# Kernel tuning notes

Hardware: AMD Instinct MI355X
Metric: run time of the kernel (lower is better)

The kernel has to match this reference:

```python
import jax, jax.numpy as jnp
import numpy as np

LOG_2PI = float(np.log(2.0 * np.pi))


def setup_inputs() -> dict:
    key = jax.random.key(0)
    k1, k2, k3 = jax.random.split(key, 3)
    B, C, D = 256, 1000, 256
    return {
        "x": jax.random.normal(k1, (B, D), dtype=jnp.float32),
        "metric_tensor": jax.random.normal(k2, (B, D, D), dtype=jnp.float32),
        "log_priors": jnp.zeros((C,), dtype=jnp.float32),
        "class_means": jax.random.normal(k3, (C, D), dtype=jnp.float32),
        "class_log_vars": jnp.zeros((C, D), dtype=jnp.float32),
    }


def reference(x, metric_tensor, log_priors, class_means, class_log_vars):
    D = x.shape[-1]
    # diff: [B, C, D]
    diff = x[:, None, :] - class_means[None, :, :]
    # Mahalanobis quadratic form per (batch, class): diff^T G diff
    maha = jnp.einsum("bcd,bde,bce->bc", diff, metric_tensor, diff)
    log_likelihood = -0.5 * (maha + jnp.sum(class_log_vars, axis=-1)[None, :] + D * LOG_2PI)
    log_posteriors = log_likelihood + log_priors[None, :]
    return jax.nn.log_softmax(log_posteriors, axis=-1)
```

## Files before the change

kernel.cpp:

```cpp
#include <hip/hip_runtime.h>

#define LOG2PI 1.83787706640934548356f

typedef __attribute__((ext_vector_type(4))) float f32x4;
typedef __attribute__((ext_vector_type(2))) float f32x2;
typedef __attribute__((ext_vector_type(8))) short bf16x8;

__device__ __forceinline__ unsigned short f2bf(float f) {
    union { float f; unsigned u; } v; v.f = f;
    unsigned r = v.u + 0x7fffu + ((v.u >> 16) & 1u);
    return (unsigned short)(r >> 16);
}
__device__ __forceinline__ float bf2f(unsigned short h) {
    union { unsigned u; float f; } v; v.u = ((unsigned)h) << 16; return v.f;
}
__device__ __forceinline__ bf16x8 pack8(f32x4 a, f32x4 b) {
    bf16x8 h;
    h[0]=(short)f2bf(a[0]); h[1]=(short)f2bf(a[1]); h[2]=(short)f2bf(a[2]); h[3]=(short)f2bf(a[3]);
    h[4]=(short)f2bf(b[0]); h[5]=(short)f2bf(b[1]); h[6]=(short)f2bf(b[2]); h[7]=(short)f2bf(b[3]);
    return h;
}
__device__ __forceinline__ float rowsum16(float v) {
    v += __int_as_float(__builtin_amdgcn_update_dpp(0, __float_as_int(v), 0x111, 0xf, 0xf, true));
    v += __int_as_float(__builtin_amdgcn_update_dpp(0, __float_as_int(v), 0x112, 0xf, 0xf, true));
    v += __int_as_float(__builtin_amdgcn_update_dpp(0, __float_as_int(v), 0x114, 0xf, 0xf, true));
    v += __int_as_float(__builtin_amdgcn_update_dpp(0, __float_as_int(v), 0x118, 0xf, 0xf, true));
    return v;
}

__global__ __launch_bounds__(256)
void k_prep(const float* __restrict__ clv, const float* __restrict__ lp,
            float* __restrict__ bias)
{
    const int w = threadIdx.x >> 6, lane = threadIdx.x & 63;
    const int c = blockIdx.x * 4 + w;
    if (c >= 1000) return;
    f32x4 v = *reinterpret_cast<const f32x4*>(clv + c * 256 + lane * 4);
    float s = v[0] + v[1] + v[2] + v[3];
    #pragma unroll
    for (int m = 1; m < 64; m <<= 1) s += __shfl_xor(s, m);
    if (lane == 0) bias[c] = lp[c] - 0.5f * (s + 256.0f * LOG2PI);
}

__global__ __launch_bounds__(512, 2)
void k_main(const float* __restrict__ x, const float* __restrict__ G,
            const float* __restrict__ means, const float* __restrict__ bias,
            float* __restrict__ out)
{
    __shared__ char dbuf[2][16384];
    __shared__ float maha[1024];
    __shared__ float red[8];

    const int b    = blockIdx.x;
    const int tid  = threadIdx.x;
    const int lane = tid & 63;
    const int wave = tid >> 6;
    const int wm   = wave >> 2;
    const int wn   = wave & 3;
    const int lrow = lane & 15;
    const int g    = lane >> 4;

    const float* Gb = G + (size_t)b * 65536;
    const float* xb = x + b * 256;

    maha[tid] = 0.f; maha[tid + 512] = 0.f;

    bf16x8 greg[4][8];
    #pragma unroll
    for (int n = 0; n < 4; ++n) {
        const float* rowp = Gb + (size_t)(wn * 64 + n * 16 + lrow) * 256 + g * 8;
        #pragma unroll
        for (int ks = 0; ks < 8; ++ks) {
            f32x4 v0 = *reinterpret_cast<const f32x4*>(rowp + ks * 32);
            f32x4 v1 = *reinterpret_cast<const f32x4*>(rowp + ks * 32 + 4);
            greg[n][ks] = pack8(v0, v1);
        }
    }

    const int sr = tid & 31;
    const int ss = tid >> 5;
    const f32x4 x0a = *reinterpret_cast<const f32x4*>(xb + ss * 8);
    const f32x4 x0b = *reinterpret_cast<const f32x4*>(xb + ss * 8 + 4);
    const f32x4 x1a = *reinterpret_cast<const f32x4*>(xb + (ss + 16) * 8);
    const f32x4 x1b = *reinterpret_cast<const f32x4*>(xb + (ss + 16) * 8 + 4);

    f32x4 r0a, r0b, r1a, r1b;
    auto load_chunk = [&](int c0) {
        int cc = c0 + sr; if (cc > 999) cc = 999;
        const float* mp = means + (size_t)cc * 256;
        r0a = *reinterpret_cast<const f32x4*>(mp + ss * 8);
        r0b = *reinterpret_cast<const f32x4*>(mp + ss * 8 + 4);
        r1a = *reinterpret_cast<const f32x4*>(mp + (ss + 16) * 8);
        r1b = *reinterpret_cast<const f32x4*>(mp + (ss + 16) * 8 + 4);
    };
    auto write_chunk = [&](int bufi) {
        *reinterpret_cast<bf16x8*>(dbuf[bufi] + (ss * 32 + sr) * 16)        = pack8(x0a - r0a, x0b - r0b);
        *reinterpret_cast<bf16x8*>(dbuf[bufi] + ((ss + 16) * 32 + sr) * 16) = pack8(x1a - r1a, x1b - r1b);
    };

    load_chunk(0);

    for (int t = 0; t < 32; ++t) {
        write_chunk(t & 1);
        __syncthreads();
        if (t < 31) load_chunk((t + 1) * 32);

        const char* buf = dbuf[t & 1];
        f32x4 acc[4];
        #pragma unroll
        for (int n = 0; n < 4; ++n) acc[n] = f32x4{0.f, 0.f, 0.f, 0.f};

        #pragma unroll
        for (int ks = 0; ks < 8; ++ks) {
            bf16x8 afr = *reinterpret_cast<const bf16x8*>(
                buf + ((ks * 4 + g) * 32 + wm * 16 + lrow) * 16);
            #pragma unroll
            for (int n = 0; n < 4; ++n)
                acc[n] = __builtin_amdgcn_mfma_f32_16x16x32_bf16(afr, greg[n][ks], acc[n], 0, 0, 0);
        }

        float p[4] = {0.f, 0.f, 0.f, 0.f};
        #pragma unroll
        for (int n = 0; n < 4; ++n) {
            const int col = wn * 64 + n * 16 + lrow;
            const char* dp = buf + ((col >> 3) * 32) * 16 + (col & 7) * 2;
            #pragma unroll
            for (int i = 0; i < 4; ++i) {
                const int row = wm * 16 + g * 4 + i;
                p[i] += acc[n][i] * bf2f(*reinterpret_cast<const unsigned short*>(dp + row * 16));
            }
        }
        #pragma unroll
        for (int i = 0; i < 4; ++i) p[i] = rowsum16(p[i]);
        if (lrow == 15) {
            const int c = t * 32 + wm * 16 + g * 4;
            #pragma unroll
            for (int i = 0; i < 4; ++i)
                if (c + i < 1000) atomicAdd(&maha[c + i], p[i]);
        }
    }

    __syncthreads();

    const int c2 = tid * 2;
    float a0 = -3.0e38f, a1 = -3.0e38f;
    if (c2 < 1000) {
        f32x2 mh = *reinterpret_cast<const f32x2*>(&maha[c2]);
        f32x2 bi = *reinterpret_cast<const f32x2*>(bias + c2);
        a0 = -0.5f * mh[0] + bi[0];
        a1 = -0.5f * mh[1] + bi[1];
    }
    float mx = fmaxf(a0, a1);
    #pragma unroll
    for (int m = 1; m < 64; m <<= 1) mx = fmaxf(mx, __shfl_xor(mx, m));
    if (lane == 0) red[wave] = mx;
    __syncthreads();
    float bm = red[0];
    #pragma unroll
    for (int i = 1; i < 8; ++i) bm = fmaxf(bm, red[i]);
    __syncthreads();
    float se = 0.f;
    if (c2 < 1000) se = expf(a0 - bm) + expf(a1 - bm);
    #pragma unroll
    for (int m = 1; m < 64; m <<= 1) se += __shfl_xor(se, m);
    if (lane == 0) red[wave] = se;
    __syncthreads();
    float ssum = red[0];
    #pragma unroll
    for (int i = 1; i < 8; ++i) ssum += red[i];
    const float lse = bm + logf(ssum);
    if (c2 < 1000) {
        f32x2 o; o[0] = a0 - lse; o[1] = a1 - lse;
        *reinterpret_cast<f32x2*>(out + (size_t)b * 1000 + c2) = o;
    }
}

extern "C" void kernel_launch(void* const* d_in, const int* in_sizes, int n_in,
                              void* d_out, int out_size, void* d_ws, size_t ws_size,
                              hipStream_t stream)
{
    const float* x     = (const float*)d_in[0];
    const float* G     = (const float*)d_in[1];
    const float* lp    = (const float*)d_in[2];
    const float* means = (const float*)d_in[3];
    const float* clv   = (const float*)d_in[4];
    float* out  = (float*)d_out;
    float* bias = (float*)d_ws;

    k_prep<<<250, 256, 0, stream>>>(clv, lp, bias);
    k_main<<<256, 512, 0, stream>>>(x, G, means, bias, out);
}
```

Baseline: 171.3 us.

## Split metric columns across two blocks per batch and move softmax to separate kernel

Each batch row is now handled by two blocks, each covering half of the output dimension of G. Per-block quadratic-form partials are atomically accumulated into a global workspace that is zeroed with a memset, and a new kernel then computes the log-softmax. The aim is to double the grid from 256 to 512 blocks and halve the per-block G register footprint, so that more blocks fit per CU (launch bounds raised from 2 to 4). In exchange, every block still rebuilds the full diff tile, and the change adds a memset, a third kernel launch, global atomics and an extra global round trip of the maha values.

```diff
diff --git a/kernel.cpp b/kernel.cpp
--- a/kernel.cpp
+++ b/kernel.cpp
@@ -42,16 +42,15 @@
     if (lane == 0) bias[c] = lp[c] - 0.5f * (s + 256.0f * LOG2PI);
 }
 
-__global__ __launch_bounds__(512, 2)
+__global__ __launch_bounds__(512, 4)
 void k_main(const float* __restrict__ x, const float* __restrict__ G,
-            const float* __restrict__ means, const float* __restrict__ bias,
-            float* __restrict__ out)
+            const float* __restrict__ means, float* __restrict__ maha_ws)
 {
     __shared__ char dbuf[2][16384];
     __shared__ float maha[1024];
-    __shared__ float red[8];
-
-    const int b    = blockIdx.x;
+
+    const int b    = blockIdx.x >> 1;
+    const int q    = blockIdx.x & 1;
     const int tid  = threadIdx.x;
     const int lane = tid & 63;
     const int wave = tid >> 6;
@@ -59,16 +58,17 @@
     const int wn   = wave & 3;
     const int lrow = lane & 15;
     const int g    = lane >> 4;
+    const int d0   = q * 128;
 
     const float* Gb = G + (size_t)b * 65536;
     const float* xb = x + b * 256;
 
     maha[tid] = 0.f; maha[tid + 512] = 0.f;
 
-    bf16x8 greg[4][8];
-    #pragma unroll
-    for (int n = 0; n < 4; ++n) {
-        const float* rowp = Gb + (size_t)(wn * 64 + n * 16 + lrow) * 256 + g * 8;
+    bf16x8 greg[2][8];
+    #pragma unroll
+    for (int n = 0; n < 2; ++n) {
+        const float* rowp = Gb + (size_t)(d0 + wn * 32 + n * 16 + lrow) * 256 + g * 8;
         #pragma unroll
         for (int ks = 0; ks < 8; ++ks) {
             f32x4 v0 = *reinterpret_cast<const f32x4*>(rowp + ks * 32);
@@ -106,23 +106,22 @@
         if (t < 31) load_chunk((t + 1) * 32);
 
         const char* buf = dbuf[t & 1];
-        f32x4 acc[4];
-        #pragma unroll
-        for (int n = 0; n < 4; ++n) acc[n] = f32x4{0.f, 0.f, 0.f, 0.f};
+        f32x4 acc[2];
+        acc[0] = f32x4{0.f, 0.f, 0.f, 0.f};
+        acc[1] = f32x4{0.f, 0.f, 0.f, 0.f};
 
         #pragma unroll
         for (int ks = 0; ks < 8; ++ks) {
             bf16x8 afr = *reinterpret_cast<const bf16x8*>(
                 buf + ((ks * 4 + g) * 32 + wm * 16 + lrow) * 16);
-            #pragma unroll
-            for (int n = 0; n < 4; ++n)
-                acc[n] = __builtin_amdgcn_mfma_f32_16x16x32_bf16(afr, greg[n][ks], acc[n], 0, 0, 0);
+            acc[0] = __builtin_amdgcn_mfma_f32_16x16x32_bf16(afr, greg[0][ks], acc[0], 0, 0, 0);
+            acc[1] = __builtin_amdgcn_mfma_f32_16x16x32_bf16(afr, greg[1][ks], acc[1], 0, 0, 0);
         }
 
         float p[4] = {0.f, 0.f, 0.f, 0.f};
         #pragma unroll
-        for (int n = 0; n < 4; ++n) {
-            const int col = wn * 64 + n * 16 + lrow;
+        for (int n = 0; n < 2; ++n) {
+            const int col = d0 + wn * 32 + n * 16 + lrow;
             const char* dp = buf + ((col >> 3) * 32) * 16 + (col & 7) * 2;
             #pragma unroll
             for (int i = 0; i < 4; ++i) {
@@ -141,37 +140,48 @@
     }
 
     __syncthreads();
-
-    const int c2 = tid * 2;
-    float a0 = -3.0e38f, a1 = -3.0e38f;
-    if (c2 < 1000) {
-        f32x2 mh = *reinterpret_cast<const f32x2*>(&maha[c2]);
-        f32x2 bi = *reinterpret_cast<const f32x2*>(bias + c2);
-        a0 = -0.5f * mh[0] + bi[0];
-        a1 = -0.5f * mh[1] + bi[1];
-    }
-    float mx = fmaxf(a0, a1);
+    for (int i = tid; i < 1000; i += 512)
+        atomicAdd(&maha_ws[(size_t)b * 1000 + i], maha[i]);
+}
+
+__global__ __launch_bounds__(256)
+void k_soft(const float* __restrict__ maha_ws, const float* __restrict__ bias,
+            float* __restrict__ out)
+{
+    __shared__ float red[4];
+    const int b = blockIdx.x, tid = threadIdx.x;
+    const int lane = tid & 63, w = tid >> 6;
+    float s[4];
+    float mx = -3.4e38f;
+    #pragma unroll
+    for (int i = 0; i < 4; ++i) {
+        const int c = tid + i * 256;
+        if (c < 1000) {
+            float v = -0.5f * maha_ws[(size_t)b * 1000 + c] + bias[c];
+            s[i] = v; mx = fmaxf(mx, v);
+        } else s[i] = -3.4e38f;
+    }
     #pragma unroll
     for (int m = 1; m < 64; m <<= 1) mx = fmaxf(mx, __shfl_xor(mx, m));
-    if (lane == 0) red[wave] = mx;
-    __syncthreads();
-    float bm = red[0];
-    #pragma unroll
-    for (int i = 1; i < 8; ++i) bm = fmaxf(bm, red[i]);
+    if (lane == 0) red[w] = mx;
+    __syncthreads();
+    const float bm = fmaxf(fmaxf(red[0], red[1]), fmaxf(red[2], red[3]));
     __syncthreads();
     float se = 0.f;
-    if (c2 < 1000) se = expf(a0 - bm) + expf(a1 - bm);
+    #pragma unroll
+    for (int i = 0; i < 4; ++i) {
+        const int c = tid + i * 256;
+        if (c < 1000) se += expf(s[i] - bm);
+    }
     #pragma unroll
     for (int m = 1; m < 64; m <<= 1) se += __shfl_xor(se, m);
-    if (lane == 0) red[wave] = se;
-    __syncthreads();
-    float ssum = red[0];
-    #pragma unroll
-    for (int i = 1; i < 8; ++i) ssum += red[i];
-    const float lse = bm + logf(ssum);
-    if (c2 < 1000) {
-        f32x2 o; o[0] = a0 - lse; o[1] = a1 - lse;
-        *reinterpret_cast<f32x2*>(out + (size_t)b * 1000 + c2) = o;
+    if (lane == 0) red[w] = se;
+    __syncthreads();
+    const float lse = bm + logf(red[0] + red[1] + red[2] + red[3]);
+    #pragma unroll
+    for (int i = 0; i < 4; ++i) {
+        const int c = tid + i * 256;
+        if (c < 1000) out[(size_t)b * 1000 + c] = s[i] - lse;
     }
 }
 
@@ -184,9 +194,12 @@
     const float* lp    = (const float*)d_in[2];
     const float* means = (const float*)d_in[3];
     const float* clv   = (const float*)d_in[4];
-    float* out  = (float*)d_out;
-    float* bias = (float*)d_ws;
-
+    float* out     = (float*)d_out;
+    float* maha_ws = (float*)d_ws;
+    float* bias    = (float*)d_ws + 256 * 1000;
+
+    hipMemsetAsync(maha_ws, 0, (size_t)256 * 1000 * sizeof(float), stream);
     k_prep<<<250, 256, 0, stream>>>(clv, lp, bias);
-    k_main<<<256, 512, 0, stream>>>(x, G, means, bias, out);
-}
+    k_main<<<512, 512, 0, stream>>>(x, G, means, maha_ws);
+    k_soft<<<256, 256, 0, stream>>>(maha_ws, bias, out);
+}
```

New measurement: 188.7 us. 10.2% more time.
